# Kernel tuning notes

Hardware: AMD Instinct MI355X
Metric: run time of the kernel (lower is better)

## Reference

```python
import jax, jax.numpy as jnp
import numpy as np

B, N, NEMBED, E, H = 4, 256, 10000, 63, 128
D = E + 1  # feature dim after concat = 64


def _lin(key, fan_in, fan_out):
    k1, k2 = jax.random.split(key)
    bound = 1.0 / np.sqrt(fan_in)
    W = jax.random.uniform(k1, (fan_in, fan_out), jnp.float32, -bound, bound)
    b = jax.random.uniform(k2, (fan_out,), jnp.float32, -bound, bound)
    return W, b


def setup_inputs() -> dict:
    key = jax.random.key(0)
    ks = jax.random.split(key, 9)
    xcat = jax.random.randint(ks[0], (B, N), 0, NEMBED, dtype=jnp.int64)
    xfeat = jax.random.normal(ks[1], (B, N), dtype=jnp.float32)
    emb = jax.random.normal(ks[2], (NEMBED, E), dtype=jnp.float32)
    W1, b1 = _lin(ks[3], D, H)
    W2, b2 = _lin(ks[4], H, H)
    W3, b3 = _lin(ks[5], H, H)
    D1, c1 = _lin(ks[6], H, H)
    D2, c2 = _lin(ks[7], H, H)
    D3, c3 = _lin(ks[8], H, 1)
    return {"xcat": xcat, "xfeat": xfeat, "emb": emb,
            "W1": W1, "b1": b1, "W2": W2, "b2": b2, "W3": W3, "b3": b3,
            "D1": D1, "c1": c1, "D2": D2, "c2": c2, "D3": D3, "c3": c3}


def reference(xcat, xfeat, emb, W1, b1, W2, b2, W3, b3, D1, c1, D2, c2, D3, c3):
    # embed + concat scalar feature -> [B, N, D]
    x = jnp.concatenate([emb[xcat], xfeat[..., None]], axis=-1)
    # pairwise outer product over the set dim -> [B, N, N, D]
    # (original: einsum 'bid,bjd->bdij' then permute(0,2,3,1) == 'bid,bjd->bijd')
    p = jnp.einsum('bid,bjd->bijd', x, x)
    # per-pair 3-layer MLP (enc)
    h = jnp.maximum(p @ W1 + b1, 0.0)
    h = jnp.maximum(h @ W2 + b2, 0.0)
    h = h @ W3 + b3
    # relu -> mean pool over (i, j) -> relu; dropout is identity in eval
    h = jnp.maximum(h, 0.0)
    h = jnp.mean(h, axis=(1, 2))  # [B, H]
    h = jnp.maximum(h, 0.0)
    # dec MLP -> [B, 1]
    h = jnp.maximum(h @ D1 + c1, 0.0)
    h = jnp.maximum(h @ D2 + c2, 0.0)
    return h @ D3 + c3
```

## Files before the change

### kernel.cpp

```cpp
#include <hip/hip_runtime.h>
#include <hip/hip_bf16.h>


#define NB 4
#define NN 256
#define HD 128
#define TPB 257

typedef __attribute__((ext_vector_type(8))) short bf16x8;
typedef __attribute__((ext_vector_type(4))) float f32x4;

__device__ __forceinline__ unsigned rne2(float a, float b) {
    unsigned ua = __builtin_bit_cast(unsigned, a);
    unsigned ub = __builtin_bit_cast(unsigned, b);
    ua = ua + 0x7fff + ((ua >> 16) & 1);
    ub = ub + 0x7fff + ((ub >> 16) & 1);
    return (ua >> 16) | (ub & 0xffff0000u);
}

__device__ __forceinline__ short f2bf(float f) {
    unsigned u = __builtin_bit_cast(unsigned, f);
    u = (u + 0x7fff + ((u >> 16) & 1)) >> 16;
    return (short)u;
}

__device__ __forceinline__ void tri_ij(int t, int& i, int& j) {
    j = (int)((sqrtf(8.0f * (float)t + 1.0f) - 1.0f) * 0.5f);
    while (((j + 1) * (j + 2) >> 1) <= t) ++j;
    while (((j * (j + 1)) >> 1) > t) --j;
    i = t - ((j * (j + 1)) >> 1);
}

__device__ __forceinline__ void pack_w(const float* __restrict__ W, short* __restrict__ pw,
                                       int KQ, int u) {
    int l  = u & 63;
    int kq = (u >> 6) % KQ;
    int mt = (u >> 6) / KQ;
    int q = l >> 4, m = l & 15;
    int c = mt * 16 + m;
#pragma unroll
    for (int j = 0; j < 8; ++j) {
        int k = kq * 32 + q * 8 + j;
        pw[u * 8 + j] = f2bf(W[k * 128 + c]);
    }
}

__global__ void prep_kernel(const int* __restrict__ xcat,
                            const float* __restrict__ xfeat,
                            const float* __restrict__ emb,
                            const float* __restrict__ W1,
                            const float* __restrict__ W2,
                            const float* __restrict__ W3,
                            float* __restrict__ x,
                            short* __restrict__ pw1,
                            short* __restrict__ pw2,
                            short* __restrict__ pw3)
{
    int bid = blockIdx.x;
    int tid = threadIdx.x;
    if (bid < 256) {
        int f = bid * 256 + tid;
        int d = f & 63;
        int nn = f >> 6;
        float v;
        if (d < 63) v = emb[xcat[nn] * 63 + d];
        else        v = xfeat[nn];
        x[f] = v;
    } else if (bid < 260) {
        pack_w(W1, pw1, 2, (bid - 256) * 256 + tid);
    } else if (bid < 268) {
        pack_w(W2, pw2, 4, (bid - 260) * 256 + tid);
    } else {
        pack_w(W3, pw3, 4, (bid - 268) * 256 + tid);
    }
}

__global__ __launch_bounds__(256, 3) void pair_mlp(
    const float* __restrict__ x,
    const short* __restrict__ pw1, const float* __restrict__ b1,
    const short* __restrict__ pw2, const float* __restrict__ b2,
    const short* __restrict__ pw3, const float* __restrict__ b3,
    float* __restrict__ partialOut)
{
    __shared__ short smP[128 * 64];
    __shared__ short smH[128 * 128];
    __shared__ float smW[128];

    const int tid = threadIdx.x;
    const int l = tid & 63;
    const int w = __builtin_amdgcn_readfirstlane(tid >> 6);
    const int wm = w >> 1;
    const int wn = w & 1;
    const int q = l >> 4;
    const int m = l & 15;
    const int b = blockIdx.y;
    const int tbase = blockIdx.x * 128;
    const float* xb = x + (b << 14);
    char* smPc = (char*)smP;
    char* smHc = (char*)smH;

    {
        const int p = tid >> 1;
        const int half = tid & 1;
        int i, j;
        tri_ij(tbase + p, i, j);
        if (half == 0) smW[p] = (i == j) ? 1.0f : 2.0f;
        const float4* xi4 = (const float4*)(xb + (i << 6) + half * 32);
        const float4* xj4 = (const float4*)(xb + (j << 6) + half * 32);
#pragma unroll
        for (int c = 0; c < 4; ++c) {
            float4 a0 = xi4[2 * c], a1 = xi4[2 * c + 1];
            float4 u0 = xj4[2 * c], u1 = xj4[2 * c + 1];
            uint4 s;
            s.x = rne2(a0.x * u0.x, a0.y * u0.y);
            s.y = rne2(a0.z * u0.z, a0.w * u0.w);
            s.z = rne2(a1.x * u1.x, a1.y * u1.y);
            s.w = rne2(a1.z * u1.z, a1.w * u1.w);
            int chunk = half * 4 + c;
            int phys = chunk ^ (p & 7);
            *(uint4*)(smPc + p * 128 + phys * 16) = s;
        }
    }
    __syncthreads();

    f32x4 acc[4][4];

#pragma unroll
    for (int mt = 0; mt < 4; ++mt) {
        float4 bv = *(const float4*)(b1 + (wm * 4 + mt) * 16 + q * 4);
        f32x4 init = {bv.x, bv.y, bv.z, bv.w};
#pragma unroll
        for (int nt = 0; nt < 4; ++nt) acc[mt][nt] = init;
    }

#pragma unroll
    for (int kq = 0; kq < 2; ++kq) {
        bf16x8 bfr[4], afr[4];
#pragma unroll
        for (int nt = 0; nt < 4; ++nt) {
            int pair = wn * 64 + nt * 16 + m;
            int phys = (kq * 4 + q) ^ (pair & 7);
            bfr[nt] = *(const bf16x8*)(smPc + pair * 128 + phys * 16);
        }
#pragma unroll
        for (int mt = 0; mt < 4; ++mt)
            afr[mt] = *(const bf16x8*)(pw1 + ((((wm * 4 + mt) * 2 + kq) * 64 + l) << 3));
#pragma unroll
        for (int mt = 0; mt < 4; ++mt)
#pragma unroll
            for (int nt = 0; nt < 4; ++nt)
                acc[mt][nt] = __builtin_amdgcn_mfma_f32_16x16x32_bf16(afr[mt], bfr[nt], acc[mt][nt], 0, 0, 0);
    }

#pragma unroll
    for (int mt = 0; mt < 4; ++mt) {
        int mtg = wm * 4 + mt;
#pragma unroll
        for (int nt = 0; nt < 4; ++nt) {
            int pair = wn * 64 + nt * 16 + m;
            uint2 sv;
            sv.x = rne2(fmaxf(acc[mt][nt][0], 0.f), fmaxf(acc[mt][nt][1], 0.f));
            sv.y = rne2(fmaxf(acc[mt][nt][2], 0.f), fmaxf(acc[mt][nt][3], 0.f));
            int chunk = mtg * 2 + (q >> 1);
            int phys = chunk ^ (pair & 15);
            *(uint2*)(smHc + pair * 256 + phys * 16 + (q & 1) * 8) = sv;
        }
    }
    __syncthreads();

#pragma unroll
    for (int mt = 0; mt < 4; ++mt) {
        float4 bv = *(const float4*)(b2 + (wm * 4 + mt) * 16 + q * 4);
        f32x4 init = {bv.x, bv.y, bv.z, bv.w};
#pragma unroll
        for (int nt = 0; nt < 4; ++nt) acc[mt][nt] = init;
    }

#pragma unroll
    for (int kq = 0; kq < 4; ++kq) {
        bf16x8 bfr[4], afr[4];
#pragma unroll
        for (int nt = 0; nt < 4; ++nt) {
            int pair = wn * 64 + nt * 16 + m;
            int phys = (kq * 4 + q) ^ (pair & 15);
            bfr[nt] = *(const bf16x8*)(smHc + pair * 256 + phys * 16);
        }
#pragma unroll
        for (int mt = 0; mt < 4; ++mt)
            afr[mt] = *(const bf16x8*)(pw2 + ((((wm * 4 + mt) * 4 + kq) * 64 + l) << 3));
#pragma unroll
        for (int mt = 0; mt < 4; ++mt)
#pragma unroll
            for (int nt = 0; nt < 4; ++nt)
                acc[mt][nt] = __builtin_amdgcn_mfma_f32_16x16x32_bf16(afr[mt], bfr[nt], acc[mt][nt], 0, 0, 0);
    }
    __syncthreads();

#pragma unroll
    for (int mt = 0; mt < 4; ++mt) {
        int mtg = wm * 4 + mt;
#pragma unroll
        for (int nt = 0; nt < 4; ++nt) {
            int pair = wn * 64 + nt * 16 + m;
            uint2 sv;
            sv.x = rne2(fmaxf(acc[mt][nt][0], 0.f), fmaxf(acc[mt][nt][1], 0.f));
            sv.y = rne2(fmaxf(acc[mt][nt][2], 0.f), fmaxf(acc[mt][nt][3], 0.f));
            int chunk = mtg * 2 + (q >> 1);
            int phys = chunk ^ (pair & 15);
            *(uint2*)(smHc + pair * 256 + phys * 16 + (q & 1) * 8) = sv;
        }
    }
    __syncthreads();

#pragma unroll
    for (int mt = 0; mt < 4; ++mt) {
        float4 bv = *(const float4*)(b3 + (wm * 4 + mt) * 16 + q * 4);
        f32x4 init = {bv.x, bv.y, bv.z, bv.w};
#pragma unroll
        for (int nt = 0; nt < 4; ++nt) acc[mt][nt] = init;
    }

#pragma unroll
    for (int kq = 0; kq < 4; ++kq) {
        bf16x8 bfr[4], afr[4];
#pragma unroll
        for (int nt = 0; nt < 4; ++nt) {
            int pair = wn * 64 + nt * 16 + m;
            int phys = (kq * 4 + q) ^ (pair & 15);
            bfr[nt] = *(const bf16x8*)(smHc + pair * 256 + phys * 16);
        }
#pragma unroll
        for (int mt = 0; mt < 4; ++mt)
            afr[mt] = *(const bf16x8*)(pw3 + ((((wm * 4 + mt) * 4 + kq) * 64 + l) << 3));
#pragma unroll
        for (int mt = 0; mt < 4; ++mt)
#pragma unroll
            for (int nt = 0; nt < 4; ++nt)
                acc[mt][nt] = __builtin_amdgcn_mfma_f32_16x16x32_bf16(afr[mt], bfr[nt], acc[mt][nt], 0, 0, 0);
    }

    float wpv[4];
#pragma unroll
    for (int nt = 0; nt < 4; ++nt)
        wpv[nt] = smW[wn * 64 + nt * 16 + m];

    float* smPart = (float*)smP;
#pragma unroll
    for (int mt = 0; mt < 4; ++mt) {
        int mtg = wm * 4 + mt;
        float vs[4];
#pragma unroll
        for (int r = 0; r < 4; ++r) {
            vs[r] = wpv[0] * fmaxf(acc[mt][0][r], 0.f) + wpv[1] * fmaxf(acc[mt][1][r], 0.f)
                  + wpv[2] * fmaxf(acc[mt][2][r], 0.f) + wpv[3] * fmaxf(acc[mt][3][r], 0.f);
#pragma unroll
            for (int s = 1; s < 16; s <<= 1)
                vs[r] += __shfl_xor(vs[r], s, 64);
        }
        if (m == 0) {
            float* p = smPart + wn * HD + mtg * 16 + q * 4;
            p[0] = vs[0]; p[1] = vs[1]; p[2] = vs[2]; p[3] = vs[3];
        }
    }
    __syncthreads();

    if (tid < HD) {
        float v = smPart[tid] + smPart[HD + tid];
        partialOut[(b * TPB + blockIdx.x) * HD + tid] = v;
    }
}

__global__ __launch_bounds__(1024) void reduce_decode(
    const float* __restrict__ partial,
    const float* __restrict__ D1, const float* __restrict__ c1,
    const float* __restrict__ D2, const float* __restrict__ c2,
    const float* __restrict__ D3, const float* __restrict__ c3,
    float* __restrict__ out)
{
    __shared__ float red8[8][HD];
    __shared__ float red2[2][HD];
    __shared__ float hb[HD];
    __shared__ float tb[HD];
    const int b = blockIdx.x;
    const int t = threadIdx.x;
    const int ch = t & 127, sl = t >> 7;

    {
        const float* base = partial + b * TPB * HD + ch;
        float s0 = 0.f, s1 = 0.f, s2 = 0.f, s3 = 0.f;
        int tl = sl;
        for (; tl + 32 <= TPB; tl += 32) {
            s0 += base[(tl     ) * HD];
            s1 += base[(tl +  8) * HD];
            s2 += base[(tl + 16) * HD];
            s3 += base[(tl + 24) * HD];
        }
        for (; tl < TPB; tl += 8) s0 += base[tl * HD];
        red8[sl][ch] = (s0 + s1) + (s2 + s3);
    }
    __syncthreads();
    if (sl == 0) {
        float v = ((red8[0][ch] + red8[1][ch]) + (red8[2][ch] + red8[3][ch]))
                + ((red8[4][ch] + red8[5][ch]) + (red8[6][ch] + red8[7][ch]));
        hb[ch] = fmaxf(v * (1.0f / 65536.0f), 0.0f);
    }
    __syncthreads();

    const int hf = sl & 1;

    if (t < 256) {
        float a = 0.f;
        for (int k = hf * 64; k < hf * 64 + 64; ++k)
            a = fmaf(hb[k], D1[(k << 7) + ch], a);
        red2[hf][ch] = a;
    }
    __syncthreads();
    if (t < 128)
        tb[ch] = fmaxf(red2[0][ch] + red2[1][ch] + c1[ch], 0.0f);
    __syncthreads();

    if (t < 256) {
        float a = 0.f;
        for (int k = hf * 64; k < hf * 64 + 64; ++k)
            a = fmaf(tb[k], D2[(k << 7) + ch], a);
        red2[hf][ch] = a;
    }
    __syncthreads();
    if (t < 128)
        hb[ch] = fmaxf(red2[0][ch] + red2[1][ch] + c2[ch], 0.0f);
    __syncthreads();

    if (t < 128) red2[0][ch] = hb[ch] * D3[ch];
    __syncthreads();
    if (t < 64) {
        float r = red2[0][t] + red2[0][t + 64];
#pragma unroll
        for (int s2 = 1; s2 < 64; s2 <<= 1)
            r += __shfl_xor(r, s2, 64);
        if (t == 0) out[b] = r + c3[0];
    }
}

extern "C" void kernel_launch(void* const* d_in, const int* in_sizes, int n_in,
                              void* d_out, int out_size, void* d_ws, size_t ws_size,
                              hipStream_t stream)
{
    (void)in_sizes; (void)n_in; (void)out_size; (void)ws_size;

    const int*   xcat  = (const int*)  d_in[0];
    const float* xfeat = (const float*)d_in[1];
    const float* emb   = (const float*)d_in[2];
    const float* W1    = (const float*)d_in[3];
    const float* b1    = (const float*)d_in[4];
    const float* W2    = (const float*)d_in[5];
    const float* b2    = (const float*)d_in[6];
    const float* W3    = (const float*)d_in[7];
    const float* b3    = (const float*)d_in[8];
    const float* D1    = (const float*)d_in[9];
    const float* c1    = (const float*)d_in[10];
    const float* D2    = (const float*)d_in[11];
    const float* c2    = (const float*)d_in[12];
    const float* D3    = (const float*)d_in[13];
    const float* c3    = (const float*)d_in[14];
    float* out = (float*)d_out;

    float* x       = (float*)d_ws;
    short* pw1     = (short*)(x + NB * NN * 64);
    short* pw2     = pw1 + 8 * 2 * 64 * 8;
    short* pw3     = pw2 + 8 * 4 * 64 * 8;
    float* partial = (float*)(pw3 + 8 * 4 * 64 * 8);

    prep_kernel<<<276, 256, 0, stream>>>(xcat, xfeat, emb, W1, W2, W3,
                                         x, pw1, pw2, pw3);
    pair_mlp<<<dim3(TPB, NB), 256, 0, stream>>>(x, pw1, b1, pw2, b2, pw3, b3, partial);
    reduce_decode<<<NB, 1024, 0, stream>>>(partial, D1, c1, D2, c2, D3, c3, out);
}
```

Measured before the change: 117.9 us.

## Switch pair MLP from bf16 to fp16 MFMA with packed conversions and pair LUT

Stores x and the packed weights as fp16, forms pair products with a vector half multiply, and converts activations with the hardware pkrtz pack instruction instead of manual bf16 rounding. It also precomputes the triangular (i,j) pair indices into a lookup table in the prep kernel, removing the per-block sqrt search. The aim is fewer ALU instructions and half the global bytes for x. The cost is fp16 range and round-toward-zero precision risk, plus more prep blocks.

```diff
diff --git a/kernel.cpp b/kernel.cpp
--- a/kernel.cpp
+++ b/kernel.cpp
@@ -1,27 +1,18 @@
 #include <hip/hip_runtime.h>
-#include <hip/hip_bf16.h>
 
 
 #define NB 4
 #define NN 256
 #define HD 128
 #define TPB 257
-
-typedef __attribute__((ext_vector_type(8))) short bf16x8;
+#define NPAIR 32896
+
+typedef _Float16 half_t;
+typedef __attribute__((ext_vector_type(8))) _Float16 half8;
 typedef __attribute__((ext_vector_type(4))) float f32x4;
 
-__device__ __forceinline__ unsigned rne2(float a, float b) {
-    unsigned ua = __builtin_bit_cast(unsigned, a);
-    unsigned ub = __builtin_bit_cast(unsigned, b);
-    ua = ua + 0x7fff + ((ua >> 16) & 1);
-    ub = ub + 0x7fff + ((ub >> 16) & 1);
-    return (ua >> 16) | (ub & 0xffff0000u);
-}
-
-__device__ __forceinline__ short f2bf(float f) {
-    unsigned u = __builtin_bit_cast(unsigned, f);
-    u = (u + 0x7fff + ((u >> 16) & 1)) >> 16;
-    return (short)u;
+__device__ __forceinline__ unsigned pkrtz(float a, float b) {
+    return __builtin_bit_cast(unsigned, __builtin_amdgcn_cvt_pkrtz(a, b));
 }
 
 __device__ __forceinline__ void tri_ij(int t, int& i, int& j) {
@@ -31,7 +22,7 @@
     i = t - ((j * (j + 1)) >> 1);
 }
 
-__device__ __forceinline__ void pack_w(const float* __restrict__ W, short* __restrict__ pw,
+__device__ __forceinline__ void pack_w(const float* __restrict__ W, half_t* __restrict__ pw,
                                        int KQ, int u) {
     int l  = u & 63;
     int kq = (u >> 6) % KQ;
@@ -41,7 +32,7 @@
 #pragma unroll
     for (int j = 0; j < 8; ++j) {
         int k = kq * 32 + q * 8 + j;
-        pw[u * 8 + j] = f2bf(W[k * 128 + c]);
+        pw[u * 8 + j] = (half_t)W[k * 128 + c];
     }
 }
 
@@ -51,10 +42,11 @@
                             const float* __restrict__ W1,
                             const float* __restrict__ W2,
                             const float* __restrict__ W3,
-                            float* __restrict__ x,
-                            short* __restrict__ pw1,
-                            short* __restrict__ pw2,
-                            short* __restrict__ pw3)
+                            half_t* __restrict__ x,
+                            half_t* __restrict__ pw1,
+                            half_t* __restrict__ pw2,
+                            half_t* __restrict__ pw3,
+                            unsigned short* __restrict__ lut)
 {
     int bid = blockIdx.x;
     int tid = threadIdx.x;
@@ -65,25 +57,33 @@
         float v;
         if (d < 63) v = emb[xcat[nn] * 63 + d];
         else        v = xfeat[nn];
-        x[f] = v;
+        x[f] = (half_t)v;
     } else if (bid < 260) {
         pack_w(W1, pw1, 2, (bid - 256) * 256 + tid);
     } else if (bid < 268) {
         pack_w(W2, pw2, 4, (bid - 260) * 256 + tid);
+    } else if (bid < 276) {
+        pack_w(W3, pw3, 4, (bid - 268) * 256 + tid);
     } else {
-        pack_w(W3, pw3, 4, (bid - 268) * 256 + tid);
+        int t = (bid - 276) * 256 + tid;
+        if (t < NPAIR) {
+            int i, j;
+            tri_ij(t, i, j);
+            lut[t] = (unsigned short)(i | (j << 8));
+        }
     }
 }
 
 __global__ __launch_bounds__(256, 3) void pair_mlp(
-    const float* __restrict__ x,
-    const short* __restrict__ pw1, const float* __restrict__ b1,
-    const short* __restrict__ pw2, const float* __restrict__ b2,
-    const short* __restrict__ pw3, const float* __restrict__ b3,
+    const half_t* __restrict__ x,
+    const unsigned short* __restrict__ lut,
+    const half_t* __restrict__ pw1, const float* __restrict__ b1,
+    const half_t* __restrict__ pw2, const float* __restrict__ b2,
+    const half_t* __restrict__ pw3, const float* __restrict__ b3,
     float* __restrict__ partialOut)
 {
-    __shared__ short smP[128 * 64];
-    __shared__ short smH[128 * 128];
+    __shared__ half_t smP[128 * 64];
+    __shared__ half_t smH[128 * 128];
     __shared__ float smW[128];
 
     const int tid = threadIdx.x;
@@ -95,30 +95,24 @@
     const int m = l & 15;
     const int b = blockIdx.y;
     const int tbase = blockIdx.x * 128;
-    const float* xb = x + (b << 14);
+    const half_t* xb = x + (b << 14);
     char* smPc = (char*)smP;
     char* smHc = (char*)smH;
 
     {
         const int p = tid >> 1;
-        const int half = tid & 1;
-        int i, j;
-        tri_ij(tbase + p, i, j);
-        if (half == 0) smW[p] = (i == j) ? 1.0f : 2.0f;
-        const float4* xi4 = (const float4*)(xb + (i << 6) + half * 32);
-        const float4* xj4 = (const float4*)(xb + (j << 6) + half * 32);
+        const int hf = tid & 1;
+        unsigned short ij = lut[tbase + p];
+        int i = ij & 255, j = ij >> 8;
+        if (hf == 0) smW[p] = (i == j) ? 1.0f : 2.0f;
+        const half8* xi = (const half8*)(xb + (i << 6) + hf * 32);
+        const half8* xj = (const half8*)(xb + (j << 6) + hf * 32);
 #pragma unroll
         for (int c = 0; c < 4; ++c) {
-            float4 a0 = xi4[2 * c], a1 = xi4[2 * c + 1];
-            float4 u0 = xj4[2 * c], u1 = xj4[2 * c + 1];
-            uint4 s;
-            s.x = rne2(a0.x * u0.x, a0.y * u0.y);
-            s.y = rne2(a0.z * u0.z, a0.w * u0.w);
-            s.z = rne2(a1.x * u1.x, a1.y * u1.y);
-            s.w = rne2(a1.z * u1.z, a1.w * u1.w);
-            int chunk = half * 4 + c;
+            half8 s = xi[c] * xj[c];
+            int chunk = hf * 4 + c;
             int phys = chunk ^ (p & 7);
-            *(uint4*)(smPc + p * 128 + phys * 16) = s;
+            *(uint4*)(smPc + p * 128 + phys * 16) = __builtin_bit_cast(uint4, s);
         }
     }
     __syncthreads();
@@ -135,21 +129,21 @@
 
 #pragma unroll
     for (int kq = 0; kq < 2; ++kq) {
-        bf16x8 bfr[4], afr[4];
+        half8 bfr[4], afr[4];
 #pragma unroll
         for (int nt = 0; nt < 4; ++nt) {
             int pair = wn * 64 + nt * 16 + m;
             int phys = (kq * 4 + q) ^ (pair & 7);
-            bfr[nt] = *(const bf16x8*)(smPc + pair * 128 + phys * 16);
-        }
-#pragma unroll
-        for (int mt = 0; mt < 4; ++mt)
-            afr[mt] = *(const bf16x8*)(pw1 + ((((wm * 4 + mt) * 2 + kq) * 64 + l) << 3));
+            bfr[nt] = *(const half8*)(smPc + pair * 128 + phys * 16);
+        }
+#pragma unroll
+        for (int mt = 0; mt < 4; ++mt)
+            afr[mt] = *(const half8*)(pw1 + ((((wm * 4 + mt) * 2 + kq) * 64 + l) << 3));
 #pragma unroll
         for (int mt = 0; mt < 4; ++mt)
 #pragma unroll
             for (int nt = 0; nt < 4; ++nt)
-                acc[mt][nt] = __builtin_amdgcn_mfma_f32_16x16x32_bf16(afr[mt], bfr[nt], acc[mt][nt], 0, 0, 0);
+                acc[mt][nt] = __builtin_amdgcn_mfma_f32_16x16x32_f16(afr[mt], bfr[nt], acc[mt][nt], 0, 0, 0);
     }
 
 #pragma unroll
@@ -159,8 +153,8 @@
         for (int nt = 0; nt < 4; ++nt) {
             int pair = wn * 64 + nt * 16 + m;
             uint2 sv;
-            sv.x = rne2(fmaxf(acc[mt][nt][0], 0.f), fmaxf(acc[mt][nt][1], 0.f));
-            sv.y = rne2(fmaxf(acc[mt][nt][2], 0.f), fmaxf(acc[mt][nt][3], 0.f));
+            sv.x = pkrtz(fmaxf(acc[mt][nt][0], 0.f), fmaxf(acc[mt][nt][1], 0.f));
+            sv.y = pkrtz(fmaxf(acc[mt][nt][2], 0.f), fmaxf(acc[mt][nt][3], 0.f));
             int chunk = mtg * 2 + (q >> 1);
             int phys = chunk ^ (pair & 15);
             *(uint2*)(smHc + pair * 256 + phys * 16 + (q & 1) * 8) = sv;
@@ -178,21 +172,21 @@
 
 #pragma unroll
     for (int kq = 0; kq < 4; ++kq) {
-        bf16x8 bfr[4], afr[4];
+        half8 bfr[4], afr[4];
 #pragma unroll
         for (int nt = 0; nt < 4; ++nt) {
             int pair = wn * 64 + nt * 16 + m;
             int phys = (kq * 4 + q) ^ (pair & 15);
-            bfr[nt] = *(const bf16x8*)(smHc + pair * 256 + phys * 16);
-        }
-#pragma unroll
-        for (int mt = 0; mt < 4; ++mt)
-            afr[mt] = *(const bf16x8*)(pw2 + ((((wm * 4 + mt) * 4 + kq) * 64 + l) << 3));
+            bfr[nt] = *(const half8*)(smHc + pair * 256 + phys * 16);
+        }
+#pragma unroll
+        for (int mt = 0; mt < 4; ++mt)
+            afr[mt] = *(const half8*)(pw2 + ((((wm * 4 + mt) * 4 + kq) * 64 + l) << 3));
 #pragma unroll
         for (int mt = 0; mt < 4; ++mt)
 #pragma unroll
             for (int nt = 0; nt < 4; ++nt)
-                acc[mt][nt] = __builtin_amdgcn_mfma_f32_16x16x32_bf16(afr[mt], bfr[nt], acc[mt][nt], 0, 0, 0);
+                acc[mt][nt] = __builtin_amdgcn_mfma_f32_16x16x32_f16(afr[mt], bfr[nt], acc[mt][nt], 0, 0, 0);
     }
     __syncthreads();
 
@@ -203,8 +197,8 @@
         for (int nt = 0; nt < 4; ++nt) {
             int pair = wn * 64 + nt * 16 + m;
             uint2 sv;
-            sv.x = rne2(fmaxf(acc[mt][nt][0], 0.f), fmaxf(acc[mt][nt][1], 0.f));
-            sv.y = rne2(fmaxf(acc[mt][nt][2], 0.f), fmaxf(acc[mt][nt][3], 0.f));
+            sv.x = pkrtz(fmaxf(acc[mt][nt][0], 0.f), fmaxf(acc[mt][nt][1], 0.f));
+            sv.y = pkrtz(fmaxf(acc[mt][nt][2], 0.f), fmaxf(acc[mt][nt][3], 0.f));
             int chunk = mtg * 2 + (q >> 1);
             int phys = chunk ^ (pair & 15);
             *(uint2*)(smHc + pair * 256 + phys * 16 + (q & 1) * 8) = sv;
@@ -222,21 +216,21 @@
 
 #pragma unroll
     for (int kq = 0; kq < 4; ++kq) {
-        bf16x8 bfr[4], afr[4];
+        half8 bfr[4], afr[4];
 #pragma unroll
         for (int nt = 0; nt < 4; ++nt) {
             int pair = wn * 64 + nt * 16 + m;
             int phys = (kq * 4 + q) ^ (pair & 15);
-            bfr[nt] = *(const bf16x8*)(smHc + pair * 256 + phys * 16);
-        }
-#pragma unroll
-        for (int mt = 0; mt < 4; ++mt)
-            afr[mt] = *(const bf16x8*)(pw3 + ((((wm * 4 + mt) * 4 + kq) * 64 + l) << 3));
+            bfr[nt] = *(const half8*)(smHc + pair * 256 + phys * 16);
+        }
+#pragma unroll
+        for (int mt = 0; mt < 4; ++mt)
+            afr[mt] = *(const half8*)(pw3 + ((((wm * 4 + mt) * 4 + kq) * 64 + l) << 3));
 #pragma unroll
         for (int mt = 0; mt < 4; ++mt)
 #pragma unroll
             for (int nt = 0; nt < 4; ++nt)
-                acc[mt][nt] = __builtin_amdgcn_mfma_f32_16x16x32_bf16(afr[mt], bfr[nt], acc[mt][nt], 0, 0, 0);
+                acc[mt][nt] = __builtin_amdgcn_mfma_f32_16x16x32_f16(afr[mt], bfr[nt], acc[mt][nt], 0, 0, 0);
     }
 
     float wpv[4];
@@ -364,14 +358,15 @@
     const float* c3    = (const float*)d_in[14];
     float* out = (float*)d_out;
 
-    float* x       = (float*)d_ws;
-    short* pw1     = (short*)(x + NB * NN * 64);
-    short* pw2     = pw1 + 8 * 2 * 64 * 8;
-    short* pw3     = pw2 + 8 * 4 * 64 * 8;
-    float* partial = (float*)(pw3 + 8 * 4 * 64 * 8);
-
-    prep_kernel<<<276, 256, 0, stream>>>(xcat, xfeat, emb, W1, W2, W3,
-                                         x, pw1, pw2, pw3);
-    pair_mlp<<<dim3(TPB, NB), 256, 0, stream>>>(x, pw1, b1, pw2, b2, pw3, b3, partial);
+    half_t* x   = (half_t*)d_ws;
+    half_t* pw1 = x + NB * NN * 64;
+    half_t* pw2 = pw1 + 8 * 2 * 64 * 8;
+    half_t* pw3 = pw2 + 8 * 4 * 64 * 8;
+    unsigned short* lut = (unsigned short*)(pw3 + 8 * 4 * 64 * 8);
+    float* partial = (float*)(lut + NPAIR);
+
+    prep_kernel<<<405, 256, 0, stream>>>(xcat, xfeat, emb, W1, W2, W3,
+                                         x, pw1, pw2, pw3, lut);
+    pair_mlp<<<dim3(TPB, NB), 256, 0, stream>>>(x, lut, pw1, b1, pw2, b2, pw3, b3, partial);
     reduce_decode<<<NB, 1024, 0, stream>>>(partial, D1, c1, D2, c2, D3, c3, out);
 }
```

New measurement: 109.4 us (median of 3 runs). 7.2% less time.
